# Kernel tuning notes

Hardware: AMD Instinct MI355X
Metric: run time of the kernel (lower is better)

Reference implementation:

```python
import jax, jax.numpy as jnp
import numpy as np

NODE_DIM = 256
HIDDEN = 256
EDGE_DIM = 128
LN_EPS = 1e-5


def setup_inputs() -> dict:
    key = jax.random.key(0)
    ks = jax.random.split(key, 5)
    B, N = 1, 512
    node = jax.random.normal(ks[0], (B, N, NODE_DIM), dtype=jnp.float32)
    ln_w = 1.0 + 0.02 * jax.random.normal(ks[1], (NODE_DIM,), dtype=jnp.float32)
    ln_b = 0.02 * jax.random.normal(ks[2], (NODE_DIM,), dtype=jnp.float32)
    proj_w = jax.random.normal(ks[3], (2 * HIDDEN, NODE_DIM), dtype=jnp.float32) / np.sqrt(NODE_DIM)
    proj_b = jnp.zeros((2 * HIDDEN,), dtype=jnp.float32)  # zero-init per module
    o_w = jax.random.normal(ks[4], (EDGE_DIM, 2 * HIDDEN), dtype=jnp.float32) / np.sqrt(2 * HIDDEN)
    o_b = jnp.zeros((EDGE_DIM,), dtype=jnp.float32)  # zero-init per module
    return {"node": node, "ln_w": ln_w, "ln_b": ln_b, "proj_w": proj_w,
            "proj_b": proj_b, "o_w": o_w, "o_b": o_b}


def _layernorm(x, w, b):
    mu = jnp.mean(x, axis=-1, keepdims=True)
    var = jnp.mean(jnp.square(x - mu), axis=-1, keepdims=True)
    return (x - mu) * jax.lax.rsqrt(var + LN_EPS) * w + b


def reference(node, ln_w, ln_b, proj_w, proj_b, o_w, o_b):
    # node: [B, N, D]
    s = _layernorm(node, ln_w, ln_b)
    s = s @ proj_w.T + proj_b                      # [B, N, 2H]
    q, k = jnp.split(s, 2, axis=-1)                # each [B, N, H]
    # prod[b,i,j,h] = q[b,j,h] * k[b,i,h]; diff[b,i,j,h] = q[b,j,h] - k[b,i,h]
    prod = q[:, None, :, :] * k[:, :, None, :]     # [B, N, N, H]
    diff = q[:, None, :, :] - k[:, :, None, :]     # [B, N, N, H]
    # cat + linear split into two GEMMs to avoid writing the [B,N,N,2H] concat
    w_p, w_d = jnp.split(o_w, 2, axis=1)           # [E, H] each
    x = jnp.einsum('bijh,eh->bije', prod, w_p) \
        + jnp.einsum('bijh,eh->bije', diff, w_d) + o_b  # [B, N, N, E]
    return x
```

## Files before the change

kernel.cpp:

```cpp
#include <hip/hip_runtime.h>

using u16 = unsigned short;
using u32 = unsigned int;

typedef __attribute__((ext_vector_type(8))) _Float16 f16x8;
typedef __attribute__((ext_vector_type(4))) float floatx4;

#define NTOK 512
#define DIM  256
#define EDIM 128

__global__ __launch_bounds__(256) void k1_ln_proj(
    const float* __restrict__ node, const float* __restrict__ ln_w,
    const float* __restrict__ ln_b, const float* __restrict__ proj_w,
    const float* __restrict__ proj_b, const float* __restrict__ o_w,
    const float* __restrict__ o_b,
    u16* __restrict__ qo, u16* __restrict__ ko,
    float* __restrict__ qdb, float* __restrict__ kdo)
{
    __shared__ float sn[4][DIM];
    __shared__ float sfull[4][2*DIM];
    const int tid  = threadIdx.x;
    const int wid  = tid >> 6;
    const int lane = tid & 63;
    const int n0   = blockIdx.x * 4;

    {
        const int n = n0 + wid;
        const int d = lane * 4;
        const float4 x = *(const float4*)(node + n*DIM + d);
        float s  = x.x + x.y + x.z + x.w;
        float ss = x.x*x.x + x.y*x.y + x.z*x.z + x.w*x.w;
        #pragma unroll
        for (int off = 32; off > 0; off >>= 1) {
            s  += __shfl_xor(s,  off);
            ss += __shfl_xor(ss, off);
        }
        const float mu   = s * (1.0f/DIM);
        const float var  = ss * (1.0f/DIM) - mu*mu;
        const float rstd = rsqrtf(var + 1e-5f);
        const float4 w = *(const float4*)(ln_w + d);
        const float4 b = *(const float4*)(ln_b + d);
        sn[wid][d+0] = (x.x-mu)*rstd*w.x + b.x;
        sn[wid][d+1] = (x.y-mu)*rstd*w.y + b.y;
        sn[wid][d+2] = (x.z-mu)*rstd*w.z + b.z;
        sn[wid][d+3] = (x.w-mu)*rstd*w.w + b.w;
    }
    __syncthreads();

    {
        const int c0 = tid, c1 = tid + DIM;
        const float bq = proj_b[c0], bk = proj_b[c1];
        float accq[4], acck[4];
        #pragma unroll
        for (int r = 0; r < 4; ++r) { accq[r] = bq; acck[r] = bk; }
        const float* w0p = proj_w + c0*DIM;
        const float* w1p = proj_w + c1*DIM;
        for (int d = 0; d < DIM; d += 4) {
            const float4 wa = *(const float4*)(w0p + d);
            const float4 wb = *(const float4*)(w1p + d);
            #pragma unroll
            for (int r = 0; r < 4; ++r) {
                const float s0 = sn[r][d+0], s1 = sn[r][d+1];
                const float s2 = sn[r][d+2], s3 = sn[r][d+3];
                accq[r] += wa.x*s0 + wa.y*s1 + wa.z*s2 + wa.w*s3;
                acck[r] += wb.x*s0 + wb.y*s1 + wb.z*s2 + wb.w*s3;
            }
        }
        #pragma unroll
        for (int r = 0; r < 4; ++r) {
            sfull[r][c0] = accq[r];
            sfull[r][c1] = acck[r];
            qo[(n0+r)*DIM + c0] = __builtin_bit_cast(u16, (_Float16)accq[r]);
            ko[(n0+r)*DIM + c0] = __builtin_bit_cast(u16, (_Float16)acck[r]);
        }
    }
    __syncthreads();

    {
        const int e    = tid & (EDIM-1);
        const int half = tid >> 7;
        const float* wd = o_w + e*(2*DIM) + DIM;
        float a[4] = {0.f, 0.f, 0.f, 0.f};
        for (int h = 0; h < DIM; h += 4) {
            const float4 w = *(const float4*)(wd + h);
            #pragma unroll
            for (int r = 0; r < 4; ++r) {
                const float* sp = &sfull[r][half*DIM + h];
                a[r] += w.x*sp[0] + w.y*sp[1] + w.z*sp[2] + w.w*sp[3];
            }
        }
        if (half == 0) {
            const float ob = o_b[e];
            #pragma unroll
            for (int r = 0; r < 4; ++r) qdb[(n0+r)*EDIM + e] = a[r] + ob;
        } else {
            #pragma unroll
            for (int r = 0; r < 4; ++r) kdo[(n0+r)*EDIM + e] = a[r];
        }
    }
}

__global__ __launch_bounds__(256, 1) void k2_edge(
    const u16* __restrict__ qg, const u16* __restrict__ kg,
    const float* __restrict__ qdb, const float* __restrict__ kdg,
    const float* __restrict__ o_w, float* __restrict__ outp)
{
    const int tid  = threadIdx.x;
    const int wid  = tid >> 6;
    const int lane = tid & 63;
    const int col  = lane & 15;
    const int quad = lane >> 4;
    const int bid  = blockIdx.x;
    const int j0 = (bid & 3) * 128 + (wid & 1) * 64;
    const int e0 = (wid >> 1) * 64;
    const int i0 = (bid >> 2) * 8;

    f16x8 bfr[4][8];
    #pragma unroll
    for (int et = 0; et < 4; ++et) {
        const float* p = o_w + (e0 + et*16 + col) * 512 + quad*8;
        #pragma unroll
        for (int ks = 0; ks < 8; ++ks) {
            const float4 lo = *(const float4*)(p + ks*32);
            const float4 hi = *(const float4*)(p + ks*32 + 4);
            f16x8 v;
            v[0] = (_Float16)lo.x; v[1] = (_Float16)lo.y;
            v[2] = (_Float16)lo.z; v[3] = (_Float16)lo.w;
            v[4] = (_Float16)hi.x; v[5] = (_Float16)hi.y;
            v[6] = (_Float16)hi.z; v[7] = (_Float16)hi.w;
            bfr[et][ks] = v;
        }
    }
    f16x8 afr[4][8];
    #pragma unroll
    for (int mt = 0; mt < 4; ++mt) {
        const u16* p = qg + (j0 + mt*16 + col) * 256 + quad*8;
        #pragma unroll
        for (int ks = 0; ks < 8; ++ks)
            afr[mt][ks] = __builtin_bit_cast(f16x8, *(const uint4*)(p + ks*32));
    }
    floatx4 qiv[4][4];
    #pragma unroll
    for (int mt = 0; mt < 4; ++mt) {
        #pragma unroll
        for (int et = 0; et < 4; ++et) {
            const int ec = e0 + et*16 + col;
            #pragma unroll
            for (int r = 0; r < 4; ++r)
                qiv[mt][et][r] = qdb[(j0 + mt*16 + quad*4 + r) * EDIM + ec];
        }
    }

    #pragma unroll 1
    for (int i = i0; i < i0 + 8; ++i) {
        float kdv[4];
        #pragma unroll
        for (int et = 0; et < 4; ++et)
            kdv[et] = kdg[i*EDIM + e0 + et*16 + col];

        floatx4 acc[4][4];
        #pragma unroll
        for (int mt = 0; mt < 4; ++mt)
            #pragma unroll
            for (int et = 0; et < 4; ++et)
                acc[mt][et] = qiv[mt][et] - kdv[et];

        const u16* kp = kg + i*256 + quad*8;
        #pragma unroll
        for (int ks = 0; ks < 8; ++ks) {
            const f16x8 kv = __builtin_bit_cast(f16x8, *(const uint4*)(kp + ks*32));
            #pragma unroll
            for (int mt = 0; mt < 4; ++mt) {
                const f16x8 sa = afr[mt][ks] * kv;
                #pragma unroll
                for (int et = 0; et < 4; ++et)
                    acc[mt][et] = __builtin_amdgcn_mfma_f32_16x16x32_f16(
                        sa, bfr[et][ks], acc[mt][et], 0, 0, 0);
            }
        }

        float* ob = outp + (size_t)i * (NTOK * EDIM);
        #pragma unroll
        for (int mt = 0; mt < 4; ++mt) {
            #pragma unroll
            for (int et = 0; et < 4; ++et) {
                const int ec = e0 + et*16 + col;
                #pragma unroll
                for (int r = 0; r < 4; ++r)
                    ob[(j0 + mt*16 + quad*4 + r) * EDIM + ec] = acc[mt][et][r];
            }
        }
    }
}

extern "C" void kernel_launch(void* const* d_in, const int* in_sizes, int n_in,
                              void* d_out, int out_size, void* d_ws, size_t ws_size,
                              hipStream_t stream) {
    const float* node   = (const float*)d_in[0];
    const float* ln_w   = (const float*)d_in[1];
    const float* ln_b   = (const float*)d_in[2];
    const float* proj_w = (const float*)d_in[3];
    const float* proj_b = (const float*)d_in[4];
    const float* o_w    = (const float*)d_in[5];
    const float* o_b    = (const float*)d_in[6];
    float* outp = (float*)d_out;

    u16*   qws = (u16*)d_ws;
    u16*   kws = qws + NTOK*DIM;
    float* qdb = (float*)(kws + NTOK*DIM);
    float* kdw = qdb + NTOK*EDIM;

    hipLaunchKernelGGL(k1_ln_proj, dim3(NTOK/4), dim3(256), 0, stream,
                       node, ln_w, ln_b, proj_w, proj_b, o_w, o_b, qws, kws, qdb, kdw);
    hipLaunchKernelGGL(k2_edge, dim3(256), dim3(256), 0, stream,
                       qws, kws, qdb, kdw, o_w, outp);
}
```

Measured before the change: 196.8 us.

## Stage q and fp16 weight tiles in shared memory and quadruple edge grid

After: 537.2 us. 2.73x slower.

```diff
diff --git a/kernel.cpp b/kernel.cpp
--- a/kernel.cpp
+++ b/kernel.cpp
@@ -15,12 +15,29 @@
     const float* __restrict__ ln_b, const float* __restrict__ proj_w,
     const float* __restrict__ proj_b, const float* __restrict__ o_w,
     const float* __restrict__ o_b,
-    u16* __restrict__ qo, u16* __restrict__ ko,
+    u16* __restrict__ qo, u16* __restrict__ ko, u16* __restrict__ wpf,
     float* __restrict__ qdb, float* __restrict__ kdo)
 {
+    const int tid = threadIdx.x;
+
+    if (blockIdx.x >= 128) {
+        const int g   = (blockIdx.x - 128) * 256 + tid;
+        const int idx = g * 8;
+        const int e   = idx >> 8;
+        const int h   = idx & 255;
+        const float4 lo = *(const float4*)(o_w + e*(2*DIM) + h);
+        const float4 hi = *(const float4*)(o_w + e*(2*DIM) + h + 4);
+        f16x8 v;
+        v[0] = (_Float16)lo.x; v[1] = (_Float16)lo.y;
+        v[2] = (_Float16)lo.z; v[3] = (_Float16)lo.w;
+        v[4] = (_Float16)hi.x; v[5] = (_Float16)hi.y;
+        v[6] = (_Float16)hi.z; v[7] = (_Float16)hi.w;
+        *(f16x8*)(wpf + idx) = v;
+        return;
+    }
+
     __shared__ float sn[4][DIM];
     __shared__ float sfull[4][2*DIM];
-    const int tid  = threadIdx.x;
     const int wid  = tid >> 6;
     const int lane = tid & 63;
     const int n0   = blockIdx.x * 4;
@@ -101,45 +118,41 @@
     }
 }
 
-__global__ __launch_bounds__(256, 1) void k2_edge(
+__global__ __launch_bounds__(256, 2) void k2_edge(
     const u16* __restrict__ qg, const u16* __restrict__ kg,
     const float* __restrict__ qdb, const float* __restrict__ kdg,
-    const float* __restrict__ o_w, float* __restrict__ outp)
+    const u16* __restrict__ wpg, float* __restrict__ outp)
 {
+    __shared__ uint4 sq4[2048];
+    __shared__ uint4 sp4[2048];
+
     const int tid  = threadIdx.x;
     const int wid  = tid >> 6;
     const int lane = tid & 63;
     const int col  = lane & 15;
     const int quad = lane >> 4;
     const int bid  = blockIdx.x;
-    const int j0 = (bid & 3) * 128 + (wid & 1) * 64;
-    const int e0 = (wid >> 1) * 64;
-    const int i0 = (bid >> 2) * 8;
-
-    f16x8 bfr[4][8];
-    #pragma unroll
-    for (int et = 0; et < 4; ++et) {
-        const float* p = o_w + (e0 + et*16 + col) * 512 + quad*8;
-        #pragma unroll
-        for (int ks = 0; ks < 8; ++ks) {
-            const float4 lo = *(const float4*)(p + ks*32);
-            const float4 hi = *(const float4*)(p + ks*32 + 4);
-            f16x8 v;
-            v[0] = (_Float16)lo.x; v[1] = (_Float16)lo.y;
-            v[2] = (_Float16)lo.z; v[3] = (_Float16)lo.w;
-            v[4] = (_Float16)hi.x; v[5] = (_Float16)hi.y;
-            v[6] = (_Float16)hi.z; v[7] = (_Float16)hi.w;
-            bfr[et][ks] = v;
-        }
-    }
-    f16x8 afr[4][8];
-    #pragma unroll
-    for (int mt = 0; mt < 4; ++mt) {
-        const u16* p = qg + (j0 + mt*16 + col) * 256 + quad*8;
-        #pragma unroll
-        for (int ks = 0; ks < 8; ++ks)
-            afr[mt][ks] = __builtin_bit_cast(f16x8, *(const uint4*)(p + ks*32));
-    }
+    const int e0 = (bid & 1) * 64;
+    const int j0 = ((bid >> 1) & 7) * 64;
+    const int i0 = (bid >> 4) * 8;
+
+    {
+        const int row   = tid >> 2;
+        const int cbase = (tid & 3) * 8;
+        const int sw    = row & 7;
+        #pragma unroll
+        for (int u = 0; u < 8; ++u) {
+            const int c = cbase + u;
+            sq4[row*32 + (c ^ sw)] = *(const uint4*)(qg  + (j0 + row)*DIM + c*8);
+            sp4[row*32 + (c ^ sw)] = *(const uint4*)(wpg + (e0 + row)*DIM + c*8);
+        }
+    }
+    __syncthreads();
+
+    const u16* sq = (const u16*)sq4;
+    const u16* sp = (const u16*)sp4;
+    const int csw = col & 7;
+
     floatx4 qiv[4][4];
     #pragma unroll
     for (int mt = 0; mt < 4; ++mt) {
@@ -153,7 +166,9 @@
     }
 
     #pragma unroll 1
-    for (int i = i0; i < i0 + 8; ++i) {
+    for (int t = 0; t < 2; ++t) {
+        const int i = i0 + wid + t*4;
+
         float kdv[4];
         #pragma unroll
         for (int et = 0; et < 4; ++et)
@@ -166,18 +181,26 @@
             for (int et = 0; et < 4; ++et)
                 acc[mt][et] = qiv[mt][et] - kdv[et];
 
-        const u16* kp = kg + i*256 + quad*8;
+        const u16* kp = kg + i*DIM + quad*8;
         #pragma unroll
         for (int ks = 0; ks < 8; ++ks) {
             const f16x8 kv = __builtin_bit_cast(f16x8, *(const uint4*)(kp + ks*32));
+            const int cs = ((ks*4 + quad) ^ csw) * 8;
+            f16x8 bf[4], sa[4];
+            #pragma unroll
+            for (int et = 0; et < 4; ++et)
+                bf[et] = *(const f16x8*)(sp + (et*16 + col)*DIM + cs);
             #pragma unroll
             for (int mt = 0; mt < 4; ++mt) {
-                const f16x8 sa = afr[mt][ks] * kv;
+                const f16x8 af = *(const f16x8*)(sq + (mt*16 + col)*DIM + cs);
+                sa[mt] = af * kv;
+            }
+            #pragma unroll
+            for (int mt = 0; mt < 4; ++mt)
                 #pragma unroll
                 for (int et = 0; et < 4; ++et)
                     acc[mt][et] = __builtin_amdgcn_mfma_f32_16x16x32_f16(
-                        sa, bfr[et][ks], acc[mt][et], 0, 0, 0);
-            }
+                        sa[mt], bf[et], acc[mt][et], 0, 0, 0);
         }
 
         float* ob = outp + (size_t)i * (NTOK * EDIM);
@@ -208,11 +231,13 @@
 
     u16*   qws = (u16*)d_ws;
     u16*   kws = qws + NTOK*DIM;
-    float* qdb = (float*)(kws + NTOK*DIM);
+    u16*   wpf = kws + NTOK*DIM;
+    float* qdb = (float*)(wpf + EDIM*DIM);
     float* kdw = qdb + NTOK*EDIM;
 
-    hipLaunchKernelGGL(k1_ln_proj, dim3(NTOK/4), dim3(256), 0, stream,
-                       node, ln_w, ln_b, proj_w, proj_b, o_w, o_b, qws, kws, qdb, kdw);
-    hipLaunchKernelGGL(k2_edge, dim3(256), dim3(256), 0, stream,
-                       qws, kws, qdb, kdw, o_w, outp);
+    hipLaunchKernelGGL(k1_ln_proj, dim3(144), dim3(256), 0, stream,
+                       node, ln_w, ln_b, proj_w, proj_b, o_w, o_b,
+                       qws, kws, wpf, qdb, kdw);
+    hipLaunchKernelGGL(k2_edge, dim3(1024), dim3(256), 0, stream,
+                       qws, kws, qdb, kdw, wpf, outp);
 }
```
